# Optimization experiments

Hardware: AMD Instinct MI355X
Metric: run time of the kernel (lower is better)

Reference implementation:

```python
import jax, jax.numpy as jnp
import numpy as np

NQ = 8
NL = 3
DIM = 2 ** NQ


def _rx(psi, w, theta):
    # theta: scalar or [B]
    B = psi.shape[0]
    t = jnp.atleast_1d(theta).astype(jnp.float32)
    c = jnp.cos(t / 2)[:, None, None].astype(jnp.complex64)
    s = (-1j * jnp.sin(t / 2))[:, None, None].astype(jnp.complex64)
    p = psi.reshape(B, 2 ** w, 2, -1)
    s0, s1 = p[:, :, 0], p[:, :, 1]
    return jnp.stack([c * s0 + s * s1, s * s0 + c * s1], axis=2).reshape(B, DIM)


def _ry(psi, w, theta):
    B = psi.shape[0]
    t = jnp.atleast_1d(theta).astype(jnp.float32)
    c = jnp.cos(t / 2)[:, None, None].astype(jnp.complex64)
    s = jnp.sin(t / 2)[:, None, None].astype(jnp.complex64)
    p = psi.reshape(B, 2 ** w, 2, -1)
    s0, s1 = p[:, :, 0], p[:, :, 1]
    return jnp.stack([c * s0 - s * s1, s * s0 + c * s1], axis=2).reshape(B, DIM)


def _rz(psi, w, theta):
    B = psi.shape[0]
    t = jnp.atleast_1d(theta).astype(jnp.float32)
    e0 = jnp.exp(-0.5j * t.astype(jnp.complex64))[:, None, None]
    e1 = jnp.exp(0.5j * t.astype(jnp.complex64))[:, None, None]
    p = psi.reshape(B, 2 ** w, 2, -1)
    return jnp.stack([e0 * p[:, :, 0], e1 * p[:, :, 1]], axis=2).reshape(B, DIM)


def _cnot(psi, c, t):
    # control c, target t (wire 0 = most significant axis)
    B = psi.shape[0]
    a, b = (c, t) if c < t else (t, c)
    p = psi.reshape(B, 2 ** a, 2, 2 ** (b - a - 1), 2, -1)
    caxis = 2 if c < t else 4
    taxis = 4 if c < t else 2
    idx = [slice(None)] * 6
    idx[caxis] = 1
    sub = p[tuple(idx)]  # control=1 slab, caxis removed
    fl_axis = taxis - (1 if taxis > caxis else 0)
    p = p.at[tuple(idx)].set(jnp.flip(sub, axis=fl_axis))
    return p.reshape(B, DIM)


# PauliZ signs per wire: [NQ, 2^NQ]
_bits = (np.arange(DIM)[None, :] >> (NQ - 1 - np.arange(NQ)[:, None])) & 1
_Z_SIGNS = jnp.asarray((1 - 2 * _bits).astype(np.float32))


def _quantum_layer(enc, qrx, qry, qrz):
    # enc: [B, NQ] encoding angles; qrx/qry/qrz: [NL, NQ] scalar params
    B = enc.shape[0]
    psi = jnp.zeros((B, DIM), jnp.complex64).at[:, 0].set(1.0)
    for i in range(NQ):
        psi = _rx(psi, i, enc[:, i])
    for l in range(NL):
        for i in range(NQ):
            psi = _rx(psi, i, qrx[l, i])
            psi = _ry(psi, i, qry[l, i])
            psi = _rz(psi, i, qrz[l, i])
        for i in range(NQ - 1):
            psi = _cnot(psi, i, i + 1)
        psi = _cnot(psi, NQ - 1, 0)
    probs = psi.real ** 2 + psi.imag ** 2  # [B, 2^NQ]
    return probs @ _Z_SIGNS.T  # [B, NQ] <Z_i>


def _critic(x, w1, b1, w2, b2, qrx, qry, qrz, w3, b3, w4, b4):
    h = jax.nn.relu(x @ w1 + b1)
    enc = h @ w2 + b2
    ex = _quantum_layer(enc, qrx, qry, qrz)
    h2 = jax.nn.relu(ex @ w3 + b3)
    return h2 @ w4 + b4


def setup_inputs() -> dict:
    key = jax.random.key(0)
    ks = jax.random.split(key, 32)
    B, OBS, ACT, H = 65536, 96, 32, 256
    D = OBS + ACT

    def lin(k, fin, fout):
        return jax.random.normal(k, (fin, fout), jnp.float32) * (1.0 / np.sqrt(fin))

    inp = {
        'state': jax.random.normal(ks[0], (B, OBS), jnp.float32),
        'action': jax.random.normal(ks[1], (B, ACT), jnp.float32),
    }
    for ci, tag in enumerate(['a', 'b']):
        o = 2 + ci * 15
        inp['w1' + tag] = lin(ks[o + 0], D, H)
        inp['b1' + tag] = jnp.zeros((H,), jnp.float32)
        inp['w2' + tag] = lin(ks[o + 1], H, NQ)
        inp['b2' + tag] = jnp.zeros((NQ,), jnp.float32)
        inp['qrx' + tag] = jax.random.normal(ks[o + 2], (NL, NQ), jnp.float32)
        inp['qry' + tag] = jax.random.normal(ks[o + 3], (NL, NQ), jnp.float32)
        inp['qrz' + tag] = jax.random.normal(ks[o + 4], (NL, NQ), jnp.float32)
        inp['w3' + tag] = lin(ks[o + 5], NQ, H)
        inp['b3' + tag] = jnp.zeros((H,), jnp.float32)
        inp['w4' + tag] = lin(ks[o + 6], H, 1)
        inp['b4' + tag] = jnp.zeros((1,), jnp.float32)
    return inp


def reference(state, action,
              w1a, b1a, w2a, b2a, qrxa, qrya, qrza, w3a, b3a, w4a, b4a,
              w1b, b1b, w2b, b2b, qrxb, qryb, qrzb, w3b, b3b, w4b, b4b):
    x = jnp.concatenate([state, action], axis=1)
    q1 = _critic(x, w1a, b1a, w2a, b2a, qrxa, qrya, qrza, w3a, b3a, w4a, b4a)
    q2 = _critic(x, w1b, b1b, w2b, b2b, qrxb, qryb, qrzb, w3b, b3b, w4b, b4b)
    return (q1, q2)
```

## Files before the change

kernel.cpp:

```cpp
#include <hip/hip_runtime.h>
#include <math.h>


typedef __attribute__((ext_vector_type(8))) short bfrag_t;
typedef __attribute__((ext_vector_type(16))) float accv_t;

__device__ __forceinline__ unsigned short f2bf(float x) {
  unsigned u = __float_as_uint(x);
  u += 0x7FFFu + ((u >> 16) & 1u);
  return (unsigned short)(u >> 16);
}
__device__ __forceinline__ float bf2f(unsigned short h) {
  return __uint_as_float(((unsigned)h) << 16);
}
__device__ __forceinline__ unsigned pack2(float a, float b) {
  return (unsigned)f2bf(a) | ((unsigned)f2bf(b) << 16);
}

struct C2 { float r, i; };
__device__ __forceinline__ C2 cmul(C2 a, C2 b){ return C2{a.r*b.r - a.i*b.i, a.r*b.i + a.i*b.r}; }
__device__ __forceinline__ C2 cadd(C2 a, C2 b){ return C2{a.r+b.r, a.i+b.i}; }

#define APPLY2(A,Bx)                                                        \
  { float ar=re[A], ai=im[A], br=re[Bx], bi=im[Bx];                         \
    re[A]  = u00r*ar - u00i*ai + u01r*br - u01i*bi;                         \
    im[A]  = u00r*ai + u00i*ar + u01r*bi + u01i*br;                         \
    re[Bx] = u10r*ar - u10i*ai + u11r*br - u11i*bi;                         \
    im[Bx] = u10r*ai + u10i*ar + u11r*bi + u11i*br; }

__global__ __launch_bounds__(256)
void prep_weights(const float* __restrict__ qrxa, const float* __restrict__ qrya,
                  const float* __restrict__ qrza,
                  const float* __restrict__ qrxb, const float* __restrict__ qryb,
                  const float* __restrict__ qrzb,
                  const float* __restrict__ w1a, const float* __restrict__ w1b,
                  const float* __restrict__ w2a, const float* __restrict__ w2b,
                  const float* __restrict__ w3a, const float* __restrict__ w3b,
                  const float* __restrict__ w4a, const float* __restrict__ w4b,
                  const float* __restrict__ b3a, const float* __restrict__ b3b,
                  unsigned short* __restrict__ Bm, unsigned short* __restrict__ Gm,
                  unsigned short* __restrict__ w1p, unsigned short* __restrict__ w2p) {
  int blk = blockIdx.x;
  int tid = threadIdx.x;
  if (blk < 128) {
    __shared__ float sg[192];
    int c = blk >> 6;
    if (tid < 24) {
      const float* qx = c ? qrxb : qrxa;
      const float* qy = c ? qryb : qrya;
      const float* qz = c ? qrzb : qrza;
      int g = tid;
      float tx = 0.5f*qx[g], ty = 0.5f*qy[g], tz = 0.5f*qz[g];
      float cx = cosf(tx), sx = sinf(tx);
      float cy = cosf(ty), sy = sinf(ty);
      float cz = cosf(tz), sz = sinf(tz);
      C2 rx00{cx,0.f}, rx01{0.f,-sx}, rx10{0.f,-sx}, rx11{cx,0.f};
      C2 m00 = cadd(cmul(C2{cy,0.f},rx00), cmul(C2{-sy,0.f},rx10));
      C2 m01 = cadd(cmul(C2{cy,0.f},rx01), cmul(C2{-sy,0.f},rx11));
      C2 m10 = cadd(cmul(C2{sy,0.f},rx00), cmul(C2{cy,0.f},rx10));
      C2 m11 = cadd(cmul(C2{sy,0.f},rx01), cmul(C2{cy,0.f},rx11));
      C2 e0{cz,-sz}, e1{cz,sz};
      C2 u00 = cmul(e0,m00), u01 = cmul(e0,m01), u10 = cmul(e1,m10), u11 = cmul(e1,m11);
      float* o = sg + g*8;
      o[0]=u00.r; o[1]=u00.i; o[2]=u01.r; o[3]=u01.i;
      o[4]=u10.r; o[5]=u10.i; o[6]=u11.r; o[7]=u11.i;
    }
    __syncthreads();
    int lane = tid & 63;
    int wid = blk*4 + (tid >> 6);
    int bcol = wid & 255;
    int p = __popc(bcol) & 3;
    float phr = (p==0) ? 1.f : ((p==2) ? -1.f : 0.f);
    float phi = (p==1) ? -1.f : ((p==3) ? 1.f : 0.f);
    float re[4], im[4];
    #pragma unroll
    for (int j = 0; j < 4; ++j) {
      int idx = 4*lane + j;
      re[j] = (idx==bcol) ? phr : 0.f;
      im[j] = (idx==bcol) ? phi : 0.f;
    }
    #pragma unroll
    for (int l = 0; l < 3; ++l) {
      #pragma unroll
      for (int q = 0; q < 8; ++q) {
        const float* u = &sg[(size_t)(l*8 + q)*8];
        float u00r=u[0],u00i=u[1],u01r=u[2],u01i=u[3];
        float u10r=u[4],u10i=u[5],u11r=u[6],u11i=u[7];
        if (q < 6) {
          int m = 5-q, mask = 1<<m;
          bool s1 = ((lane >> m) & 1) != 0;
          float udr = s1?u11r:u00r, udi = s1?u11i:u00i;
          float uor = s1?u10r:u01r, uoi = s1?u10i:u01i;
          #pragma unroll
          for (int j = 0; j < 4; ++j) {
            float pr = __shfl_xor(re[j], mask);
            float pi = __shfl_xor(im[j], mask);
            float nr = udr*re[j] - udi*im[j] + uor*pr - uoi*pi;
            float ni = udr*im[j] + udi*re[j] + uor*pi + uoi*pr;
            re[j]=nr; im[j]=ni;
          }
        } else if (q == 6) { APPLY2(0,2); APPLY2(1,3); }
        else               { APPLY2(0,1); APPLY2(2,3); }
      }
      #pragma unroll
      for (int cq = 0; cq <= 4; ++cq) {
        int tmask = 1 << (4-cq);
        bool pred = ((lane >> (5-cq)) & 1) != 0;
        #pragma unroll
        for (int j = 0; j < 4; ++j) {
          float sr = __shfl_xor(re[j], tmask);
          float si = __shfl_xor(im[j], tmask);
          re[j] = pred ? sr : re[j];
          im[j] = pred ? si : im[j];
        }
      }
      { bool pred = (lane & 1) != 0;
        float t0, t1;
        t0 = pred?re[2]:re[0]; t1 = pred?re[0]:re[2]; re[0]=t0; re[2]=t1;
        t0 = pred?im[2]:im[0]; t1 = pred?im[0]:im[2]; im[0]=t0; im[2]=t1;
        t0 = pred?re[3]:re[1]; t1 = pred?re[1]:re[3]; re[1]=t0; re[3]=t1;
        t0 = pred?im[3]:im[1]; t1 = pred?im[1]:im[3]; im[1]=t0; im[3]=t1; }
      { float t;
        t=re[2]; re[2]=re[3]; re[3]=t;
        t=im[2]; im[2]=im[3]; im[3]=t; }
      { re[1]=__shfl_xor(re[1],32); im[1]=__shfl_xor(im[1],32);
        re[3]=__shfl_xor(re[3],32); im[3]=__shfl_xor(im[3],32); }
    }
    #pragma unroll
    for (int j = 0; j < 4; ++j) {
      int i = 4*lane + j;
      Bm[(size_t)(c*512 + i)*256 + bcol]       = f2bf(re[j]);
      Bm[(size_t)(c*512 + 256 + i)*256 + bcol] = f2bf(im[j]);
    }
  } else if (blk < 192) {
    int slot = (blk-128)*256 + tid;
    int n = slot & 255, h5 = (slot>>8)&1, ks = (slot>>9)&7, p = (slot>>12)&1, c = slot>>13;
    const float* w1c = c ? w1b : w1a;
    #pragma unroll
    for (int j = 0; j < 8; ++j) {
      float v = w1c[(size_t)(ks*16 + h5*8 + j)*256 + n];
      unsigned short hi = f2bf(v);
      w1p[(size_t)slot*8 + j] = p ? f2bf(v - bf2f(hi)) : hi;
    }
  } else if (blk < 200) {
    int slot = (blk-192)*256 + tid;
    int combo = slot >> 4, part = slot & 15;
    int h5 = combo&1, k16 = (combo>>1)&15, p = (combo>>5)&1, c = (combo>>6)&1;
    const float* w2c = c ? w2b : w2a;
    #pragma unroll
    for (int jj = 0; jj < 16; ++jj) {
      int idx = part*16 + jj;
      int il = idx >> 3, j = idx & 7;
      int n = k16*16 + h5*8 + j;
      float v = (il < 8) ? w2c[(size_t)n*8 + il] : 0.f;
      unsigned short hi = f2bf(v);
      w2p[(size_t)combo*256 + idx] = p ? f2bf(v - bf2f(hi)) : hi;
    }
  } else {
    int idx = (blk-200)*256 + tid;
    int j = idx & 7, lane = (idx >> 3) & 63, w = (idx >> 9) & 7, c = (idx >> 12) & 1;
    int h5 = lane >> 5, il = lane & 31;
    int n = 32*w + il;
    const float* w3 = c ? w3b : w3a;
    const float* w4 = c ? w4b : w4a;
    const float* b3 = c ? b3b : b3a;
    float aw = fabsf(w4[n]);
    float v;
    if (h5 == 0)     v = w3[(size_t)j*256 + n] * aw;
    else if (j == 0) v = b3[n] * aw;
    else             v = 0.f;
    Gm[idx] = f2bf(v);
  }
}

__global__ __launch_bounds__(256, 4)
void enc_mfma(const float* __restrict__ state, const float* __restrict__ action,
              const unsigned short* __restrict__ w1p,
              const float* __restrict__ b1a, const float* __restrict__ b1b,
              const unsigned short* __restrict__ w2p,
              const float* __restrict__ b2a, const float* __restrict__ b2b,
              float* __restrict__ enc, int Bn) {
  __shared__ __align__(16) char Bx[2][8192];
  __shared__ __align__(16) float sb1[2][256];
  __shared__ float sb2[2][8];
  __shared__ __align__(16) float encw[4][32][8];
  int tid = threadIdx.x;
  int lane = tid & 63, w = tid >> 6, il = lane & 31, h5 = lane >> 5;
  int r0 = blockIdx.x * 32;

  sb1[0][tid] = b1a[tid];
  sb1[1][tid] = b1b[tid];
  if (tid < 8) { sb2[0][tid] = b2a[tid]; sb2[1][tid] = b2b[tid]; }

  {
    int m = tid >> 3, q8 = tid & 7;
    const float4* st4 = (const float4*)state;
    const float4* ac4 = (const float4*)action;
    #pragma unroll
    for (int j = 0; j < 4; ++j) {
      int f = j*8 + q8;
      int ks = f >> 2, kq = f & 3;
      float4 v = (ks < 6) ? st4[(size_t)(r0+m)*24 + ks*4 + kq]
                          : ac4[(size_t)(r0+m)*8 + (ks-6)*4 + kq];
      unsigned short hx = f2bf(v.x), hy = f2bf(v.y), hz = f2bf(v.z), hw = f2bf(v.w);
      uint2 hh, ll;
      hh.x = (unsigned)hx | ((unsigned)hy << 16);
      hh.y = (unsigned)hz | ((unsigned)hw << 16);
      ll.x = (unsigned)f2bf(v.x - bf2f(hx)) | ((unsigned)f2bf(v.y - bf2f(hy)) << 16);
      ll.y = (unsigned)f2bf(v.z - bf2f(hz)) | ((unsigned)f2bf(v.w - bf2f(hw)) << 16);
      int off = ks*1024 + m*32 + kq*8;
      *(uint2*)(&Bx[0][off]) = hh;
      *(uint2*)(&Bx[1][off]) = ll;
    }
  }
  __syncthreads();

  for (int c = 0; c < 2; ++c) {
    accv_t A[2] = {{},{}};
    #pragma unroll
    for (int ks = 0; ks < 8; ++ks) {
      bfrag_t a0h, a0l, a1h, a1l;
      {
        size_t b0 = ((size_t)((c*2+0)*8 + ks)*2 + h5)*256;
        size_t b1 = ((size_t)((c*2+1)*8 + ks)*2 + h5)*256;
        int t0 = 2*w, t1 = 2*w+1;
        a0h = *(const bfrag_t*)(w1p + (b0 + t0*32 + il)*8);
        a0l = *(const bfrag_t*)(w1p + (b1 + t0*32 + il)*8);
        a1h = *(const bfrag_t*)(w1p + (b0 + t1*32 + il)*8);
        a1l = *(const bfrag_t*)(w1p + (b1 + t1*32 + il)*8);
      }
      bfrag_t b0h = *(const bfrag_t*)(&Bx[0][ks*1024 + il*32 + h5*16]);
      bfrag_t b0l = *(const bfrag_t*)(&Bx[1][ks*1024 + il*32 + h5*16]);
      A[0] = __builtin_amdgcn_mfma_f32_32x32x16_bf16(a0h, b0h, A[0], 0,0,0);
      A[0] = __builtin_amdgcn_mfma_f32_32x32x16_bf16(a0h, b0l, A[0], 0,0,0);
      A[0] = __builtin_amdgcn_mfma_f32_32x32x16_bf16(a0l, b0h, A[0], 0,0,0);
      A[1] = __builtin_amdgcn_mfma_f32_32x32x16_bf16(a1h, b0h, A[1], 0,0,0);
      A[1] = __builtin_amdgcn_mfma_f32_32x32x16_bf16(a1h, b0l, A[1], 0,0,0);
      A[1] = __builtin_amdgcn_mfma_f32_32x32x16_bf16(a1l, b0h, A[1], 0,0,0);
    }
    #pragma unroll
    for (int nt = 0; nt < 2; ++nt) {
      #pragma unroll
      for (int g = 0; g < 4; ++g) {
        float4 bb = *(const float4*)&sb1[c][(2*w+nt)*32 + 8*g + 4*h5];
        float bba[4] = {bb.x, bb.y, bb.z, bb.w};
        #pragma unroll
        for (int jj = 0; jj < 4; ++jj) {
          A[nt][4*g+jj] = fmaxf(A[nt][4*g+jj] + bba[jj], 0.f);
        }
      }
    }
    accv_t Cm = {};
    #pragma unroll
    for (int k2 = 0; k2 < 4; ++k2) {
      int k16 = 4*w + k2;
      bfrag_t g2h = *(const bfrag_t*)(w2p + ((size_t)((c*2+0)*16 + k16)*2 + h5)*256 + il*8);
      bfrag_t g2l = *(const bfrag_t*)(w2p + ((size_t)((c*2+1)*16 + k16)*2 + h5)*256 + il*8);
      unsigned ph[2][2], pl[2][2];
      #pragma unroll
      for (int gi = 0; gi < 2; ++gi) {
        int G = 2*k2 + gi, nt = G >> 2, g = G & 3;
        float f0 = A[nt][4*g+0], f1 = A[nt][4*g+1];
        float f2 = A[nt][4*g+2], f3 = A[nt][4*g+3];
        unsigned short h0 = f2bf(f0), h1 = f2bf(f1), h2 = f2bf(f2), h3 = f2bf(f3);
        ph[gi][0] = (unsigned)h0 | ((unsigned)h1 << 16);
        ph[gi][1] = (unsigned)h2 | ((unsigned)h3 << 16);
        pl[gi][0] = (unsigned)f2bf(f0 - bf2f(h0)) | ((unsigned)f2bf(f1 - bf2f(h1)) << 16);
        pl[gi][1] = (unsigned)f2bf(f2 - bf2f(h2)) | ((unsigned)f2bf(f3 - bf2f(h3)) << 16);
      }
      union { bfrag_t v; unsigned u[4]; } FH, FL;
      #pragma unroll
      for (int r = 0; r < 2; ++r) {
        unsigned own_h = h5 ? ph[1][r] : ph[0][r];
        unsigned alt_h = h5 ? ph[0][r] : ph[1][r];
        unsigned rec_h = __shfl_xor((int)alt_h, 32);
        FH.u[r]   = h5 ? rec_h : own_h;
        FH.u[2+r] = h5 ? own_h : rec_h;
        unsigned own_l = h5 ? pl[1][r] : pl[0][r];
        unsigned alt_l = h5 ? pl[0][r] : pl[1][r];
        unsigned rec_l = __shfl_xor((int)alt_l, 32);
        FL.u[r]   = h5 ? rec_l : own_l;
        FL.u[2+r] = h5 ? own_l : rec_l;
      }
      Cm = __builtin_amdgcn_mfma_f32_32x32x16_bf16(g2h, FH.v, Cm, 0,0,0);
      Cm = __builtin_amdgcn_mfma_f32_32x32x16_bf16(g2h, FL.v, Cm, 0,0,0);
      Cm = __builtin_amdgcn_mfma_f32_32x32x16_bf16(g2l, FH.v, Cm, 0,0,0);
    }
    *(float4*)&encw[w][il][4*h5] = make_float4(Cm[0], Cm[1], Cm[2], Cm[3]);
    __syncthreads();
    {
      int e = tid & 7, mm = tid >> 3;
      float v = sb2[c][e];
      #pragma unroll
      for (int ww = 0; ww < 4; ++ww) v += encw[ww][mm][e];
      enc[((size_t)c*Bn + r0 + mm)*8 + e] = v;
    }
    __syncthreads();
  }
}

__device__ __forceinline__ void a_build(float4 ea, float4 eb, char* Ab, int ag2, int am) {
  float c0,s0,c1,s1,c2,s2,c3,s3,c4,s4,c5,s5,c6,s6,c7,s7;
  __sincosf(0.5f*ea.x, &s0, &c0);
  __sincosf(0.5f*ea.y, &s1, &c1);
  __sincosf(0.5f*ea.z, &s2, &c2);
  __sincosf(0.5f*ea.w, &s3, &c3);
  __sincosf(0.5f*eb.x, &s4, &c4);
  __sincosf(0.5f*eb.y, &s5, &c5);
  __sincosf(0.5f*eb.z, &s6, &c6);
  __sincosf(0.5f*eb.w, &s7, &c7);
  float v0 = (ag2&8) ? s0 : c0;
  float v1 = (ag2&4) ? s1 : c1;
  float v2 = (ag2&2) ? s2 : c2;
  float v3 = (ag2&1) ? s3 : c3;
  float top = v0*v1*v2*v3;
  float hA = top*c4, hB = top*s4;
  float p67[4];
  p67[0] = c6*c7; p67[1] = c6*s7; p67[2] = s6*c7; p67[3] = s6*s7;
  float low[8];
  #pragma unroll
  for (int j = 0; j < 8; ++j) low[j] = ((j&4) ? s5 : c5) * p67[j&3];
  union { bfrag_t v; unsigned u[4]; } pk;
  #pragma unroll
  for (int k = 0; k < 4; ++k) pk.u[k] = pack2(hA*low[2*k], hA*low[2*k+1]);
  *(bfrag_t*)(Ab + ag2*1024 + am*16) = pk.v;
  #pragma unroll
  for (int k = 0; k < 4; ++k) pk.u[k] = pack2(hB*low[2*k], hB*low[2*k+1]);
  *(bfrag_t*)(Ab + ag2*1024 + 512 + am*16) = pk.v;
}

__global__ __launch_bounds__(512, 2)
void qgemm(const float* __restrict__ enc,
           const unsigned short* __restrict__ Bm, const unsigned short* __restrict__ Gm,
           const float* __restrict__ b3a, const float* __restrict__ w4a, const float* __restrict__ b4a,
           const float* __restrict__ b3b, const float* __restrict__ w4b, const float* __restrict__ b4b,
           float* __restrict__ out, int Bn) {
  __shared__ __align__(16) char APq[56576];
  char* A0 = APq;
  char* A1 = APq + 16384;
  float* exw = (float*)(APq + 32768);
  float* exf = (float*)(APq + 51200);
  float* qp  = (float*)(APq + 54272);

  int tid = threadIdx.x;
  int lane = tid & 63;
  int w = tid >> 6;
  int il = lane & 31;
  int h5 = lane >> 5;

  int c = blockIdx.x >> 7;
  int rowblock = blockIdx.x & 127;
  int rowsPerBlock = Bn >> 7;
  int npairs = rowsPerBlock >> 6;

  bfrag_t bf0[16], bf1[16];
  {
    const unsigned short* base = Bm + ((size_t)(c*512 + 32*w + il)*256 + h5*8);
    #pragma unroll
    for (int ks = 0; ks < 16; ++ks) {
      bf0[ks] = *(const bfrag_t*)(base + ks*16);
      bf1[ks] = *(const bfrag_t*)(base + 256*256 + ks*16);
    }
  }
  bfrag_t gf2 = *(const bfrag_t*)(Gm + ((size_t)((c*8 + w)*64 + lane))*8);

  int n2 = 32*w + il;
  const float* w4c = c ? w4b : w4a;
  const float* b4c = c ? b4b : b4a;
  float w4v = w4c[n2];
  float b4v = b4c[0];
  unsigned smask = (unsigned)__ballot(w4v < 0.f);

  int am = tid & 31, ag2 = tid >> 5;
  const float* encb = enc + ((size_t)c*Bn)*8;
  int rbase = rowblock*rowsPerBlock;

  {
    const float* ep0 = encb + (size_t)(rbase + am)*8;
    float4 pa0 = *(const float4*)ep0, pb0 = *(const float4*)(ep0 + 4);
    const float* ep1 = encb + (size_t)(rbase + 32 + am)*8;
    float4 pa1 = *(const float4*)ep1, pb1 = *(const float4*)(ep1 + 4);
    a_build(pa0, pb0, A0, ag2, am);
    a_build(pa1, pb1, A1, ag2, am);
  }
  __syncthreads();

  for (int st2 = 0; st2 < npairs; ++st2) {
    int r0 = rbase + st2*64;
    #pragma unroll
    for (int sub = 0; sub < 2; ++sub) {
      const char* Asel = sub ? A1 : A0;
      accv_t acc0 = {}, acc1 = {};
      #pragma unroll
      for (int ks = 0; ks < 16; ++ks) {
        bfrag_t af = *(const bfrag_t*)(Asel + ks*1024 + lane*16);
        acc0 = __builtin_amdgcn_mfma_f32_32x32x16_bf16(bf0[ks], af, acc0, 0, 0, 0);
        acc1 = __builtin_amdgcn_mfma_f32_32x32x16_bf16(bf1[ks], af, acc1, 0, 0, 0);
      }
      float Pv[16];
      #pragma unroll
      for (int r = 0; r < 16; ++r) Pv[r] = acc0[r]*acc0[r] + acc1[r]*acc1[r];
      float E  = ((Pv[0]+Pv[1])+(Pv[2]+Pv[3])) + ((Pv[4]+Pv[5])+(Pv[6]+Pv[7]));
      float S4 = ((Pv[8]+Pv[9])+(Pv[10]+Pv[11])) + ((Pv[12]+Pv[13])+(Pv[14]+Pv[15]));
      float T  = E + S4;
      float S0 = ((Pv[1]+Pv[3])+(Pv[5]+Pv[7])) + ((Pv[9]+Pv[11])+(Pv[13]+Pv[15]));
      float S1 = ((Pv[2]+Pv[3])+(Pv[6]+Pv[7])) + ((Pv[10]+Pv[11])+(Pv[14]+Pv[15]));
      float S3 = ((Pv[4]+Pv[5])+(Pv[6]+Pv[7])) + ((Pv[12]+Pv[13])+(Pv[14]+Pv[15]));
      float e[8];
      e[7] = T - 2.f*S0;
      e[6] = T - 2.f*S1;
      e[5] = h5 ? -T : T;
      e[4] = T - 2.f*S3;
      e[3] = T - 2.f*S4;
      e[2] = (w&1) ? -T : T;
      e[1] = (w&2) ? -T : T;
      e[0] = (w&4) ? -T : T;
      #pragma unroll
      for (int q = 0; q < 8; ++q) e[q] += __shfl_xor(e[q], 32);
      if (h5 == 0) {
        float* dst = exw + sub*2304 + w*288 + il*9;
        #pragma unroll
        for (int q = 0; q < 8; ++q) dst[q] = e[q];
      }
    }
    __syncthreads();
    if (st2 > 0 && tid < 64) {
      const float* qr = qp + tid*9;
      float s = ((qr[0]+qr[1]) + (qr[2]+qr[3])) + ((qr[4]+qr[5]) + (qr[6]+qr[7]));
      out[(size_t)c*Bn + (r0 - 64) + tid] = s + b4v;
    }
    float4 na0, nb0, na1, nb1;
    bool more = (st2 + 1 < npairs);
    if (more) {
      const float* ep0 = encb + (size_t)(r0 + 64 + am)*8;
      na0 = *(const float4*)ep0; nb0 = *(const float4*)(ep0 + 4);
      const float* ep1 = encb + (size_t)(r0 + 96 + am)*8;
      na1 = *(const float4*)ep1; nb1 = *(const float4*)(ep1 + 4);
    }
    {
      int sub = tid >> 8, m = (tid >> 3) & 31, q = tid & 7;
      const float* ew = exw + sub*2304 + m*9 + q;
      float s = ((ew[0] + ew[288]) + (ew[2*288] + ew[3*288]))
              + ((ew[4*288] + ew[5*288]) + (ew[6*288] + ew[7*288]));
      exf[sub*384 + m*12 + q] = s;
    }
    if (more) {
      a_build(na0, nb0, A0, ag2, am);
      a_build(na1, nb1, A1, ag2, am);
    }
    __syncthreads();
    {
      union { bfrag_t v; unsigned u[4]; } fa, fb;
      if (h5 == 0) {
        const float* e0 = exf + il*12;
        float4 x0 = *(const float4*)(e0);
        float4 x1 = *(const float4*)(e0 + 4);
        fa.u[0] = pack2(x0.x, x0.y); fa.u[1] = pack2(x0.z, x0.w);
        fa.u[2] = pack2(x1.x, x1.y); fa.u[3] = pack2(x1.z, x1.w);
        const float* e1 = exf + 384 + il*12;
        float4 y0 = *(const float4*)(e1);
        float4 y1 = *(const float4*)(e1 + 4);
        fb.u[0] = pack2(y0.x, y0.y); fb.u[1] = pack2(y0.z, y0.w);
        fb.u[2] = pack2(y1.x, y1.y); fb.u[3] = pack2(y1.z, y1.w);
      } else {
        fa.u[0] = 0x00003F80u; fa.u[1]=0; fa.u[2]=0; fa.u[3]=0;
        fb.u[0] = 0x00003F80u; fb.u[1]=0; fb.u[2]=0; fb.u[3]=0;
      }
      accv_t acc2a = {}, acc2b = {};
      acc2a = __builtin_amdgcn_mfma_f32_32x32x16_bf16(gf2, fa.v, acc2a, 0, 0, 0);
      acc2b = __builtin_amdgcn_mfma_f32_32x32x16_bf16(gf2, fb.v, acc2b, 0, 0, 0);
      float qa = 0.f, qb = 0.f;
      #pragma unroll
      for (int r = 0; r < 16; ++r) {
        int bi = (r&3) + 8*(r>>2);
        float ta = fmaxf(acc2a[r], 0.f);
        float tb = fmaxf(acc2b[r], 0.f);
        bool neg = ((smask >> (bi + 4*h5)) & 1u) != 0u;
        qa += neg ? -ta : ta;
        qb += neg ? -tb : tb;
      }
      qa += __shfl_xor(qa, 32);
      qb += __shfl_xor(qb, 32);
      if (h5 == 0) {
        qp[il*9 + w]        = qa;
        qp[(32 + il)*9 + w] = qb;
      }
    }
  }
  __syncthreads();
  if (tid < 64) {
    const float* qr = qp + tid*9;
    float s = ((qr[0]+qr[1]) + (qr[2]+qr[3])) + ((qr[4]+qr[5]) + (qr[6]+qr[7]));
    out[(size_t)c*Bn + rbase + (npairs-1)*64 + tid] = s + b4v;
  }
}

extern "C" void kernel_launch(void* const* d_in, const int* in_sizes, int n_in,
                              void* d_out, int out_size, void* d_ws, size_t ws_size,
                              hipStream_t stream) {
  (void)n_in; (void)out_size; (void)ws_size;
  const float* state  = (const float*)d_in[0];
  const float* action = (const float*)d_in[1];
  const float* w1a=(const float*)d_in[2];  const float* b1a=(const float*)d_in[3];
  const float* w2a=(const float*)d_in[4];  const float* b2a=(const float*)d_in[5];
  const float* qrxa=(const float*)d_in[6]; const float* qrya=(const float*)d_in[7];
  const float* qrza=(const float*)d_in[8];
  const float* w3a=(const float*)d_in[9];  const float* b3a=(const float*)d_in[10];
  const float* w4a=(const float*)d_in[11]; const float* b4a=(const float*)d_in[12];
  const float* w1b=(const float*)d_in[13]; const float* b1b=(const float*)d_in[14];
  const float* w2b=(const float*)d_in[15]; const float* b2b=(const float*)d_in[16];
  const float* qrxb=(const float*)d_in[17];const float* qryb=(const float*)d_in[18];
  const float* qrzb=(const float*)d_in[19];
  const float* w3b=(const float*)d_in[20]; const float* b3b=(const float*)d_in[21];
  const float* w4b=(const float*)d_in[22]; const float* b4b=(const float*)d_in[23];

  int B = in_sizes[0] / 96;
  char* wsb = (char*)d_ws;
  unsigned short* Bmat = (unsigned short*)(wsb);
  unsigned short* Gmat = (unsigned short*)(wsb + 524288);
  unsigned short* w1p  = (unsigned short*)(wsb + 786432);
  unsigned short* w2p  = (unsigned short*)(wsb + 1048576);
  float* enc           = (float*)(wsb + 1114112);

  prep_weights<<<232, 256, 0, stream>>>(qrxa,qrya,qrza,qrxb,qryb,qrzb,
                                        w1a,w1b,w2a,w2b,w3a,w3b,w4a,w4b,b3a,b3b,
                                        Bmat,Gmat,w1p,w2p);
  enc_mfma<<<B/32, 256, 0, stream>>>(state,action,w1p,b1a,b1b,w2p,b2a,b2b,enc,B);
  qgemm<<<256, 512, 0, stream>>>(enc, Bmat, Gmat, b3a, w4a, b4a, b3b, w4b, b4b,
                                 (float*)d_out, B);
}
```

Measured before the change: 203.0 us.

## Process 128 rows per iteration with four A subtiles and packed bf16 exchange

Each main-loop iteration now builds and consumes four 32-row A tiles instead of two, so the block handles 128 rows between barrier pairs. This halves the number of __syncthreads and loop-control rounds per row. The reduced feature vectors are also packed to bf16 when written to shared memory, so the second GEMM reads one 16-byte fragment instead of converting floats. In exchange, shared memory roughly doubles to about 111 KB, which prevents two blocks from sharing a CU. It also requires rows per block to be a multiple of 128.

```diff
diff --git a/kernel.cpp b/kernel.cpp
--- a/kernel.cpp
+++ b/kernel.cpp
@@ -335,12 +335,11 @@
            const float* __restrict__ b3a, const float* __restrict__ w4a, const float* __restrict__ b4a,
            const float* __restrict__ b3b, const float* __restrict__ w4b, const float* __restrict__ b4b,
            float* __restrict__ out, int Bn) {
-  __shared__ __align__(16) char APq[56576];
-  char* A0 = APq;
-  char* A1 = APq + 16384;
-  float* exw = (float*)(APq + 32768);
-  float* exf = (float*)(APq + 51200);
-  float* qp  = (float*)(APq + 54272);
+  __shared__ __align__(16) char APq[111104];
+  char* Abase = APq;
+  float* exw = (float*)(APq + 65536);
+  unsigned* exf = (unsigned*)(APq + 102400);
+  float* qp  = (float*)(APq + 106496);
 
   int tid = threadIdx.x;
   int lane = tid & 63;
@@ -351,7 +350,7 @@
   int c = blockIdx.x >> 7;
   int rowblock = blockIdx.x & 127;
   int rowsPerBlock = Bn >> 7;
-  int npairs = rowsPerBlock >> 6;
+  int niter = rowsPerBlock >> 7;
 
   bfrag_t bf0[16], bf1[16];
   {
@@ -375,21 +374,19 @@
   const float* encb = enc + ((size_t)c*Bn)*8;
   int rbase = rowblock*rowsPerBlock;
 
-  {
-    const float* ep0 = encb + (size_t)(rbase + am)*8;
-    float4 pa0 = *(const float4*)ep0, pb0 = *(const float4*)(ep0 + 4);
-    const float* ep1 = encb + (size_t)(rbase + 32 + am)*8;
-    float4 pa1 = *(const float4*)ep1, pb1 = *(const float4*)(ep1 + 4);
-    a_build(pa0, pb0, A0, ag2, am);
-    a_build(pa1, pb1, A1, ag2, am);
+  #pragma unroll
+  for (int sub = 0; sub < 4; ++sub) {
+    const float* ep = encb + (size_t)(rbase + sub*32 + am)*8;
+    float4 pa = *(const float4*)ep, pb = *(const float4*)(ep + 4);
+    a_build(pa, pb, Abase + sub*16384, ag2, am);
   }
   __syncthreads();
 
-  for (int st2 = 0; st2 < npairs; ++st2) {
-    int r0 = rbase + st2*64;
-    #pragma unroll
-    for (int sub = 0; sub < 2; ++sub) {
-      const char* Asel = sub ? A1 : A0;
+  for (int st = 0; st < niter; ++st) {
+    int r0 = rbase + st*128;
+    #pragma unroll
+    for (int sub = 0; sub < 4; ++sub) {
+      const char* Asel = Abase + sub*16384;
       accv_t acc0 = {}, acc1 = {};
       #pragma unroll
       for (int ks = 0; ks < 16; ++ks) {
@@ -424,74 +421,58 @@
       }
     }
     __syncthreads();
-    if (st2 > 0 && tid < 64) {
+    if (st > 0 && tid < 128) {
       const float* qr = qp + tid*9;
       float s = ((qr[0]+qr[1]) + (qr[2]+qr[3])) + ((qr[4]+qr[5]) + (qr[6]+qr[7]));
-      out[(size_t)c*Bn + (r0 - 64) + tid] = s + b4v;
-    }
-    float4 na0, nb0, na1, nb1;
-    bool more = (st2 + 1 < npairs);
+      out[(size_t)c*Bn + (r0 - 128) + tid] = s + b4v;
+    }
+    {
+      int sub = tid >> 7, m = (tid >> 2) & 31, k2 = tid & 3;
+      const float* ew0 = exw + sub*2304 + m*9 + 2*k2;
+      float s0 = ((ew0[0] + ew0[288]) + (ew0[2*288] + ew0[3*288]))
+               + ((ew0[4*288] + ew0[5*288]) + (ew0[6*288] + ew0[7*288]));
+      const float* ew1 = ew0 + 1;
+      float s1 = ((ew1[0] + ew1[288]) + (ew1[2*288] + ew1[3*288]))
+               + ((ew1[4*288] + ew1[5*288]) + (ew1[6*288] + ew1[7*288]));
+      exf[sub*256 + m*8 + k2] = pack2(s0, s1);
+    }
+    bool more = (st + 1 < niter);
     if (more) {
-      const float* ep0 = encb + (size_t)(r0 + 64 + am)*8;
-      na0 = *(const float4*)ep0; nb0 = *(const float4*)(ep0 + 4);
-      const float* ep1 = encb + (size_t)(r0 + 96 + am)*8;
-      na1 = *(const float4*)ep1; nb1 = *(const float4*)(ep1 + 4);
-    }
-    {
-      int sub = tid >> 8, m = (tid >> 3) & 31, q = tid & 7;
-      const float* ew = exw + sub*2304 + m*9 + q;
-      float s = ((ew[0] + ew[288]) + (ew[2*288] + ew[3*288]))
-              + ((ew[4*288] + ew[5*288]) + (ew[6*288] + ew[7*288]));
-      exf[sub*384 + m*12 + q] = s;
-    }
-    if (more) {
-      a_build(na0, nb0, A0, ag2, am);
-      a_build(na1, nb1, A1, ag2, am);
+      #pragma unroll
+      for (int sub = 0; sub < 4; ++sub) {
+        const float* ep = encb + (size_t)(r0 + 128 + sub*32 + am)*8;
+        float4 pa = *(const float4*)ep, pb = *(const float4*)(ep + 4);
+        a_build(pa, pb, Abase + sub*16384, ag2, am);
+      }
     }
     __syncthreads();
-    {
-      union { bfrag_t v; unsigned u[4]; } fa, fb;
+    #pragma unroll
+    for (int sub = 0; sub < 4; ++sub) {
+      union { bfrag_t v; unsigned u[4]; } fa;
       if (h5 == 0) {
-        const float* e0 = exf + il*12;
-        float4 x0 = *(const float4*)(e0);
-        float4 x1 = *(const float4*)(e0 + 4);
-        fa.u[0] = pack2(x0.x, x0.y); fa.u[1] = pack2(x0.z, x0.w);
-        fa.u[2] = pack2(x1.x, x1.y); fa.u[3] = pack2(x1.z, x1.w);
-        const float* e1 = exf + 384 + il*12;
-        float4 y0 = *(const float4*)(e1);
-        float4 y1 = *(const float4*)(e1 + 4);
-        fb.u[0] = pack2(y0.x, y0.y); fb.u[1] = pack2(y0.z, y0.w);
-        fb.u[2] = pack2(y1.x, y1.y); fb.u[3] = pack2(y1.z, y1.w);
+        fa.v = *(const bfrag_t*)(exf + sub*256 + il*8);
       } else {
         fa.u[0] = 0x00003F80u; fa.u[1]=0; fa.u[2]=0; fa.u[3]=0;
-        fb.u[0] = 0x00003F80u; fb.u[1]=0; fb.u[2]=0; fb.u[3]=0;
-      }
-      accv_t acc2a = {}, acc2b = {};
-      acc2a = __builtin_amdgcn_mfma_f32_32x32x16_bf16(gf2, fa.v, acc2a, 0, 0, 0);
-      acc2b = __builtin_amdgcn_mfma_f32_32x32x16_bf16(gf2, fb.v, acc2b, 0, 0, 0);
-      float qa = 0.f, qb = 0.f;
+      }
+      accv_t acc2 = {};
+      acc2 = __builtin_amdgcn_mfma_f32_32x32x16_bf16(gf2, fa.v, acc2, 0, 0, 0);
+      float qa = 0.f;
       #pragma unroll
       for (int r = 0; r < 16; ++r) {
         int bi = (r&3) + 8*(r>>2);
-        float ta = fmaxf(acc2a[r], 0.f);
-        float tb = fmaxf(acc2b[r], 0.f);
+        float ta = fmaxf(acc2[r], 0.f);
         bool neg = ((smask >> (bi + 4*h5)) & 1u) != 0u;
         qa += neg ? -ta : ta;
-        qb += neg ? -tb : tb;
       }
       qa += __shfl_xor(qa, 32);
-      qb += __shfl_xor(qb, 32);
-      if (h5 == 0) {
-        qp[il*9 + w]        = qa;
-        qp[(32 + il)*9 + w] = qb;
-      }
+      if (h5 == 0) qp[(sub*32 + il)*9 + w] = qa;
     }
   }
   __syncthreads();
-  if (tid < 64) {
+  if (tid < 128) {
     const float* qr = qp + tid*9;
     float s = ((qr[0]+qr[1]) + (qr[2]+qr[3])) + ((qr[4]+qr[5]) + (qr[6]+qr[7]));
-    out[(size_t)c*Bn + rbase + (npairs-1)*64 + tid] = s + b4v;
+    out[(size_t)c*Bn + rbase + (niter-1)*128 + tid] = s + b4v;
   }
 }
 
```

Measured after the change: 198.6 us. -2.2%, faster.
